# Kernel tuning notes

Hardware: AMD Instinct MI355X
Metric: run time of the kernel (lower is better)

## Reference

```python
import jax, jax.numpy as jnp
import numpy as np

N_NODES = 100000
N_EDGES = 3200000
IN_CH = 128
HID = 128
ACT_DIM = 1


def _gcn_layer(x, W, b, src, dst, ew, n):
    # GCNConv with edge weights and self-loops already included in (src, dst, ew).
    # Symmetric normalization: norm_e = d^{-1/2}[src] * w_e * d^{-1/2}[dst]
    h = x @ W                                            # [N, F_out] dense transform first (cheap)
    deg = jax.ops.segment_sum(ew, dst, num_segments=n)   # weighted in-degree
    dinv = jnp.where(deg > 0, jax.lax.rsqrt(deg), 0.0)
    norm = dinv[src] * ew * dinv[dst]                    # [E]
    out = jax.ops.segment_sum(norm[:, None] * h[src], dst, num_segments=n)
    return out + b


def setup_inputs() -> dict:
    key = jax.random.key(0)
    ks = jax.random.split(key, 10)
    x = jax.random.normal(ks[0], (N_NODES, IN_CH), dtype=jnp.float32)
    edge_index = jax.random.randint(ks[1], (2, N_EDGES), 0, N_NODES, dtype=jnp.int64)
    edge_weight = jax.random.uniform(ks[2], (N_EDGES,), dtype=jnp.float32)
    action = jax.random.normal(ks[3], (N_NODES, ACT_DIM), dtype=jnp.float32)
    s1 = 1.0 / np.sqrt(IN_CH)
    s2 = 1.0 / np.sqrt(HID)
    s3 = 1.0 / np.sqrt(HID + ACT_DIM)
    W1 = jax.random.uniform(ks[4], (IN_CH, HID), jnp.float32, -s1, s1)
    b1 = jnp.zeros((HID,), jnp.float32)
    W2 = jax.random.uniform(ks[5], (HID, HID), jnp.float32, -s2, s2)
    b2 = jnp.zeros((HID,), jnp.float32)
    Wfc = jax.random.uniform(ks[6], (HID + ACT_DIM, 1), jnp.float32, -s3, s3)
    bfc = jax.random.uniform(ks[7], (1,), jnp.float32, -s3, s3)
    return {"x": x, "edge_index": edge_index, "edge_weight": edge_weight,
            "action": action, "W1": W1, "b1": b1, "W2": W2, "b2": b2,
            "Wfc": Wfc, "bfc": bfc}


def reference(x, edge_index, edge_weight, action, W1, b1, W2, b2, Wfc, bfc):
    n = x.shape[0]
    loop = jnp.arange(n, dtype=edge_index.dtype)
    src = jnp.concatenate([edge_index[0], loop])          # add self-loops
    dst = jnp.concatenate([edge_index[1], loop])
    ew = jnp.concatenate([edge_weight, jnp.ones((n,), edge_weight.dtype)])

    h = jax.nn.relu(_gcn_layer(x, W1, b1, src, dst, ew, n))
    h = jax.nn.relu(_gcn_layer(h, W2, b2, src, dst, ew, n))
    h = jnp.concatenate([h, action], axis=1)              # [N, HID+ACT_DIM]
    value = (h @ Wfc + bfc).squeeze()                     # [N]
    return value
```

## Files before the change

kernel.cpp:

```cpp
#include <hip/hip_runtime.h>
#include <hip/hip_bf16.h>
#include <stdint.h>

typedef unsigned short u16;
typedef uint32_t u32;
typedef unsigned long long u64;

__device__ __forceinline__ float bf2f(u16 u) {
    return __uint_as_float(((uint32_t)u) << 16);
}
__device__ __forceinline__ u16 f2bf(float f) {
    uint32_t u = __float_as_uint(f);
    uint32_t r = u + 0x7fffu + ((u >> 16) & 1u);
    return (u16)(r >> 16);
}

__device__ __forceinline__ float ldf(const float* p) { return *p; }
__device__ __forceinline__ float ldf(const u16* p) { return bf2f(*p); }

#define DEG_SCALE 4294967296.0f
#define DEG_INV 2.3283064365386963e-10f

#define BSHIFT 9
#define BSIZE 512
#define CAP 19456

__global__ void k_init0(u32* bwptr, int NB) {
    int t = threadIdx.x;
    if (t < NB) bwptr[t] = (u32)t * CAP;
}

template <typename TIn>
__device__ __forceinline__ void gemm_block(float* smem, const TIn* __restrict__ A,
                                           const float* __restrict__ W,
                                           u16* __restrict__ outp, int n, int bid) {
    float (*As)[128] = (float(*)[128])smem;
    float (*Ws)[128] = (float(*)[128])(smem + 32 * 128);
    int t = threadIdx.x;
    int row0 = bid * 32;

    if constexpr (sizeof(TIn) == 2) {
        for (int i = t; i < 32 * 64; i += 256) {
            int r = i >> 6, c2 = i & 63;
            int gr = row0 + r;
            uint32_t u = (gr < n) ? *reinterpret_cast<const uint32_t*>(&A[(size_t)gr * 128 + 2 * c2]) : 0u;
            As[r][2 * c2] = bf2f((u16)(u & 0xffff));
            As[r][2 * c2 + 1] = bf2f((u16)(u >> 16));
        }
    } else {
        for (int i = t; i < 32 * 128; i += 256) {
            int r = i >> 7, c = i & 127;
            int gr = row0 + r;
            As[r][c] = (gr < n) ? ldf(&A[(size_t)gr * 128 + c]) : 0.0f;
        }
    }

    float acc[4][4];
#pragma unroll
    for (int i = 0; i < 4; i++)
#pragma unroll
        for (int j = 0; j < 4; j++) acc[i][j] = 0.0f;

    int c0 = (t & 31) * 4;
    int r0 = (t >> 5) * 4;

    for (int kt = 0; kt < 128; kt += 32) {
        __syncthreads();
        for (int i = t; i < 32 * 128; i += 256) {
            int kk = i >> 7, c = i & 127;
            Ws[kk][c] = W[(size_t)(kt + kk) * 128 + c];
        }
        __syncthreads();
#pragma unroll
        for (int kk = 0; kk < 32; kk += 4) {
            float w0[4], w1[4], w2[4], w3[4];
            *(float4*)w0 = *(const float4*)&Ws[kk + 0][c0];
            *(float4*)w1 = *(const float4*)&Ws[kk + 1][c0];
            *(float4*)w2 = *(const float4*)&Ws[kk + 2][c0];
            *(float4*)w3 = *(const float4*)&Ws[kk + 3][c0];
#pragma unroll
            for (int i = 0; i < 4; i++) {
                float a[4];
                *(float4*)a = *(const float4*)&As[r0 + i][kt + kk];
#pragma unroll
                for (int j = 0; j < 4; j++) {
                    acc[i][j] = fmaf(a[0], w0[j], acc[i][j]);
                    acc[i][j] = fmaf(a[1], w1[j], acc[i][j]);
                    acc[i][j] = fmaf(a[2], w2[j], acc[i][j]);
                    acc[i][j] = fmaf(a[3], w3[j], acc[i][j]);
                }
            }
        }
    }

#pragma unroll
    for (int i = 0; i < 4; i++) {
        int gr = row0 + r0 + i;
        if (gr < n) {
            ushort4 o;
            o.x = f2bf(acc[i][0]);
            o.y = f2bf(acc[i][1]);
            o.z = f2bf(acc[i][2]);
            o.w = f2bf(acc[i][3]);
            *reinterpret_cast<ushort4*>(&outp[(size_t)gr * 128 + c0]) = o;
        }
    }
}

__global__ __launch_bounds__(256) void k_part_gemm(const float* __restrict__ x, const float* __restrict__ W1,
                                                   u16* __restrict__ tbuf, int n, int Gg,
                                                   const int* __restrict__ src, const int* __restrict__ dst,
                                                   const float* __restrict__ ew,
                                                   u32* bwptr, u64* __restrict__ ebuf,
                                                   int E, int EPB, int NB) {
    __shared__ float smem[2 * 32 * 128];
    int bid = blockIdx.x;
    int g = bid / 5;
    int r = bid - g * 5;
    if (r < 3) {
        int gb = 3 * g + r;
        if (gb < Gg) gemm_block<float>(smem, x, W1, tbuf, n, gb);
        return;
    }
    int pb = 2 * g + (r - 3);
    u32* hist = (u32*)smem;
    u32* base = (u32*)smem + 256;
    int t = threadIdx.x;
    if (t < NB) hist[t] = 0;
    __syncthreads();
    int e0 = pb * EPB;
    int e1 = min(e0 + EPB, E);
    if (e0 >= E) return;
    for (int e = e0 + t; e < e1; e += 256) {
        atomicAdd(&hist[dst[e] >> BSHIFT], 1u);
    }
    __syncthreads();
    if (t < NB) {
        base[t] = atomicAdd(&bwptr[t], hist[t]);
        hist[t] = 0;
    }
    __syncthreads();
    for (int e = e0 + t; e < e1; e += 256) {
        int d = dst[e];
        int b = d >> BSHIFT;
        u32 pos = base[b] + atomicAdd(&hist[b], 1u);
        u32 w0 = (u32)src[e] | ((u32)(d & (BSIZE - 1)) << 17);
        ebuf[pos] = (u64)w0 | ((u64)__float_as_uint(ew[e]) << 32);
    }
}

__global__ __launch_bounds__(512) void k_bdegcnt(const u64* __restrict__ ebuf, const u32* __restrict__ bwptr,
                                                 u64* __restrict__ packed, int n) {
    __shared__ u64 acc[BSIZE];
    int b = blockIdx.x;
    int t = threadIdx.x;
    for (int i = t; i < BSIZE; i += 512) acc[i] = 0;
    __syncthreads();
    int cnt = (int)(bwptr[b] - (u32)b * CAP);
    const u64* eb = ebuf + (size_t)b * CAP;
    for (int e = t; e < cnt; e += 512) {
        u64 w = eb[e];
        int dlow = ((u32)w >> 17) & (BSIZE - 1);
        float wv = __uint_as_float((u32)(w >> 32));
        atomicAdd(&acc[dlow], (1ull << 48) | (u64)(wv * DEG_SCALE));
    }
    __syncthreads();
    int node0 = b << BSHIFT;
    for (int i = t; i < BSIZE; i += 512) {
        int node = node0 + i;
        if (node < n) packed[node] = acc[i] + (1ull << 32);
    }
}

__global__ void k_dinv_scan(const u64* __restrict__ packed, float* dinv, int* rowptr, int* bsum, int n) {
    __shared__ int s[256];
    int t = threadIdx.x;
    int i = blockIdx.x * 256 + t;
    u64 pk = (i < n) ? packed[i] : 0;
    if (i < n) {
        float deg = (float)(pk & 0xFFFFFFFFFFFFull) * DEG_INV;
        dinv[i] = rsqrtf(deg);
    }
    int v = (int)(pk >> 48);
    s[t] = v;
    __syncthreads();
    for (int off = 1; off < 256; off <<= 1) {
        int x = (t >= off) ? s[t - off] : 0;
        __syncthreads();
        s[t] += x;
        __syncthreads();
    }
    if (i < n) rowptr[i] = s[t] - v;
    if (t == 255) bsum[blockIdx.x] = s[255];
}

__global__ void k_scan_sums(int* bsum, int nb) {
    __shared__ int s[512];
    int t = threadIdx.x;
    int v = (t < nb) ? bsum[t] : 0;
    s[t] = v;
    __syncthreads();
    for (int off = 1; off < 512; off <<= 1) {
        int x = (t >= off) ? s[t - off] : 0;
        __syncthreads();
        s[t] += x;
        __syncthreads();
    }
    if (t < nb) bsum[t] = s[t] - v;
}

__global__ void k_scan_add(int* rowptr, const int* __restrict__ bsum, int n) {
    int i = blockIdx.x * 256 + threadIdx.x;
    if (i < n) rowptr[i] += bsum[blockIdx.x];
}

__global__ __launch_bounds__(512) void k_bscatter(const u64* __restrict__ ebuf, const u32* __restrict__ bwptr,
                                                  const int* __restrict__ rowptr, const float* __restrict__ dinv,
                                                  int2* __restrict__ rec, int n) {
    __shared__ u32 fill[BSIZE];
    __shared__ int rp[BSIZE];
    __shared__ float din[BSIZE];
    int b = blockIdx.x;
    int t = threadIdx.x;
    int node0 = b << BSHIFT;
    for (int i = t; i < BSIZE; i += 512) {
        int node = node0 + i;
        fill[i] = 0;
        rp[i] = (node < n) ? rowptr[node] : 0;
        din[i] = (node < n) ? dinv[node] : 0.f;
    }
    __syncthreads();
    int cnt = (int)(bwptr[b] - (u32)b * CAP);
    const u64* eb = ebuf + (size_t)b * CAP;
    for (int e = t; e < cnt; e += 512) {
        u64 w = eb[e];
        u32 lo = (u32)w;
        int s = lo & 0x1FFFF;
        int dlow = (lo >> 17) & (BSIZE - 1);
        float ewv = __uint_as_float((u32)(w >> 32));
        float nrm = dinv[s] * ewv * din[dlow];
        int pos = rp[dlow] + (int)atomicAdd(&fill[dlow], 1u);
        rec[pos] = make_int2(s, __float_as_int(nrm));
    }
}

template <typename TIn>
__global__ __launch_bounds__(256) void k_gemm(const TIn* __restrict__ A, const float* __restrict__ W,
                                              u16* __restrict__ outp, int n) {
    __shared__ float smem[2 * 32 * 128];
    gemm_block<TIn>(smem, A, W, outp, n, blockIdx.x);
}

template <int MODE>
__global__ __launch_bounds__(256) void k_agg(const u16* __restrict__ t, const int2* __restrict__ rec,
                                             const int* __restrict__ rowptr, const u64* __restrict__ packed,
                                             const float* __restrict__ dinv, const float* __restrict__ bias,
                                             u16* __restrict__ hout,
                                             const float* __restrict__ action, const float* __restrict__ Wfc,
                                             const float* __restrict__ bfc, float* __restrict__ out, int n) {
    int node = blockIdx.x * 4 + (threadIdx.x >> 6);
    if (node >= n) return;
    int lane = threadIdx.x & 63;
    int half = lane >> 5;
    int c4 = (lane & 31) * 4;
    int base = rowptr[node];
    int m = (int)(packed[node] >> 48);

    float4 acc = make_float4(0.f, 0.f, 0.f, 0.f);
    int e = 0;
    for (; e + 8 <= m; e += 8) {
        int2 r0 = rec[base + e + 0 + half];
        int2 r1 = rec[base + e + 2 + half];
        int2 r2 = rec[base + e + 4 + half];
        int2 r3 = rec[base + e + 6 + half];
        ushort4 g0 = *reinterpret_cast<const ushort4*>(&t[(size_t)r0.x * 128 + c4]);
        ushort4 g1 = *reinterpret_cast<const ushort4*>(&t[(size_t)r1.x * 128 + c4]);
        ushort4 g2 = *reinterpret_cast<const ushort4*>(&t[(size_t)r2.x * 128 + c4]);
        ushort4 g3 = *reinterpret_cast<const ushort4*>(&t[(size_t)r3.x * 128 + c4]);
        float n0 = __int_as_float(r0.y), n1 = __int_as_float(r1.y);
        float n2 = __int_as_float(r2.y), n3 = __int_as_float(r3.y);
        acc.x = fmaf(n0, bf2f(g0.x), acc.x); acc.y = fmaf(n0, bf2f(g0.y), acc.y);
        acc.z = fmaf(n0, bf2f(g0.z), acc.z); acc.w = fmaf(n0, bf2f(g0.w), acc.w);
        acc.x = fmaf(n1, bf2f(g1.x), acc.x); acc.y = fmaf(n1, bf2f(g1.y), acc.y);
        acc.z = fmaf(n1, bf2f(g1.z), acc.z); acc.w = fmaf(n1, bf2f(g1.w), acc.w);
        acc.x = fmaf(n2, bf2f(g2.x), acc.x); acc.y = fmaf(n2, bf2f(g2.y), acc.y);
        acc.z = fmaf(n2, bf2f(g2.z), acc.z); acc.w = fmaf(n2, bf2f(g2.w), acc.w);
        acc.x = fmaf(n3, bf2f(g3.x), acc.x); acc.y = fmaf(n3, bf2f(g3.y), acc.y);
        acc.z = fmaf(n3, bf2f(g3.z), acc.z); acc.w = fmaf(n3, bf2f(g3.w), acc.w);
    }
    for (; e + 2 <= m; e += 2) {
        int2 r = rec[base + e + half];
        ushort4 g = *reinterpret_cast<const ushort4*>(&t[(size_t)r.x * 128 + c4]);
        float nn = __int_as_float(r.y);
        acc.x = fmaf(nn, bf2f(g.x), acc.x); acc.y = fmaf(nn, bf2f(g.y), acc.y);
        acc.z = fmaf(nn, bf2f(g.z), acc.z); acc.w = fmaf(nn, bf2f(g.w), acc.w);
    }
    if (e < m && half == 0) {
        int2 r = rec[base + e];
        ushort4 g = *reinterpret_cast<const ushort4*>(&t[(size_t)r.x * 128 + c4]);
        float nn = __int_as_float(r.y);
        acc.x = fmaf(nn, bf2f(g.x), acc.x); acc.y = fmaf(nn, bf2f(g.y), acc.y);
        acc.z = fmaf(nn, bf2f(g.z), acc.z); acc.w = fmaf(nn, bf2f(g.w), acc.w);
    }
    acc.x += __shfl_xor(acc.x, 32);
    acc.y += __shfl_xor(acc.y, 32);
    acc.z += __shfl_xor(acc.z, 32);
    acc.w += __shfl_xor(acc.w, 32);

    if (half == 0) {
        float di = dinv[node];
        float sdi = di * di;
        ushort4 sv = *reinterpret_cast<const ushort4*>(&t[(size_t)node * 128 + c4]);
        acc.x = fmaf(sdi, bf2f(sv.x), acc.x);
        acc.y = fmaf(sdi, bf2f(sv.y), acc.y);
        acc.z = fmaf(sdi, bf2f(sv.z), acc.z);
        acc.w = fmaf(sdi, bf2f(sv.w), acc.w);
        float4 b = *reinterpret_cast<const float4*>(&bias[c4]);
        acc.x = fmaxf(acc.x + b.x, 0.0f);
        acc.y = fmaxf(acc.y + b.y, 0.0f);
        acc.z = fmaxf(acc.z + b.z, 0.0f);
        acc.w = fmaxf(acc.w + b.w, 0.0f);
        if (MODE == 0) {
            ushort4 o;
            o.x = f2bf(acc.x); o.y = f2bf(acc.y); o.z = f2bf(acc.z); o.w = f2bf(acc.w);
            *reinterpret_cast<ushort4*>(&hout[(size_t)node * 128 + c4]) = o;
        } else {
            float4 w = *reinterpret_cast<const float4*>(&Wfc[c4]);
            float v = acc.x * w.x + acc.y * w.y + acc.z * w.z + acc.w * w.w;
#pragma unroll
            for (int off = 16; off >= 1; off >>= 1) v += __shfl_down(v, off, 32);
            if (lane == 0) out[node] = v + action[node] * Wfc[128] + bfc[0];
        }
    }
}

extern "C" void kernel_launch(void* const* d_in, const int* in_sizes, int n_in,
                              void* d_out, int out_size, void* d_ws, size_t ws_size,
                              hipStream_t stream) {
    const float* x = (const float*)d_in[0];
    const int* ei = (const int*)d_in[1];
    const float* ew = (const float*)d_in[2];
    const float* action = (const float*)d_in[3];
    const float* W1 = (const float*)d_in[4];
    const float* b1 = (const float*)d_in[5];
    const float* W2 = (const float*)d_in[6];
    const float* b2 = (const float*)d_in[7];
    const float* Wfc = (const float*)d_in[8];
    const float* bfc = (const float*)d_in[9];
    float* out = (float*)d_out;

    int n = in_sizes[0] / 128;
    int E = in_sizes[2];
    const int* src = ei;
    const int* dst = ei + E;

    char* p = (char*)d_ws;
    auto carve = [&](size_t bytes) -> char* {
        char* q = p;
        p += (bytes + 255) & ~(size_t)255;
        return q;
    };
    int NB = (n + BSIZE - 1) >> BSHIFT;
    u64* packed = (u64*)carve((size_t)n * 8);
    float* dinv = (float*)carve((size_t)n * 4);
    int* rowptr = (int*)carve((size_t)n * 4);
    int* bsum = (int*)carve(1024 * 4);
    u32* bwptr = (u32*)carve((size_t)NB * 4);
    u64* ebuf = (u64*)carve((size_t)NB * CAP * 8);
    int2* rec = (int2*)carve(((size_t)E + 16) * 8);
    u16* tbuf = (u16*)carve((size_t)n * 128 * 2);
    u16* hbuf = (u16*)carve((size_t)n * 128 * 2);

    int nb = (n + 255) / 256;
    int Gg = (n + 31) / 32;
    int G = (Gg + 2) / 3;
    int Gp = 2 * G;
    int EPB = (E + Gp - 1) / Gp;

    k_init0<<<1, 256, 0, stream>>>(bwptr, NB);
    k_part_gemm<<<G * 5, 256, 0, stream>>>(x, W1, tbuf, n, Gg, src, dst, ew,
                                           bwptr, ebuf, E, EPB, NB);
    k_bdegcnt<<<NB, 512, 0, stream>>>(ebuf, bwptr, packed, n);
    k_dinv_scan<<<nb, 256, 0, stream>>>(packed, dinv, rowptr, bsum, n);
    k_scan_sums<<<1, 512, 0, stream>>>(bsum, nb);
    k_scan_add<<<nb, 256, 0, stream>>>(rowptr, bsum, n);
    k_bscatter<<<NB, 512, 0, stream>>>(ebuf, bwptr, rowptr, dinv, rec, n);

    k_agg<0><<<(n + 3) / 4, 256, 0, stream>>>(tbuf, rec, rowptr, packed, dinv, b1, hbuf,
                                              nullptr, nullptr, nullptr, nullptr, n);
    k_gemm<u16><<<(n + 31) / 32, 256, 0, stream>>>(hbuf, W2, tbuf, n);
    k_agg<1><<<(n + 3) / 4, 256, 0, stream>>>(tbuf, rec, rowptr, packed, dinv, b2, nullptr,
                                              action, Wfc, bfc, out, n);
}
```

Measured before the change: 561.3 us.

## Fuse degree count with per-bucket scan and widen aggregation gathers to 16 bytes

Every block of the partition kernel now does both a GEMM tile and an edge partition chunk, replacing the interleaved 3:2 block split. Degree counting, dinv and the rowptr scan are merged into one per-bucket kernel whose rowptr uses bucket-local offsets (b*CAP), so three scan kernels and the global prefix sum go away. The rec array is sized per bucket to match. The aggregation kernel now gives each lane 8 channels with 16-byte loads and processes 4 edges per step in parallel, which cuts the per-edge instruction count and the index-load overhead but adds a cross-lane reduction.

```diff
diff --git a/kernel.cpp b/kernel.cpp
--- a/kernel.cpp
+++ b/kernel.cpp
@@ -115,46 +115,45 @@
                                                    int E, int EPB, int NB) {
     __shared__ float smem[2 * 32 * 128];
     int bid = blockIdx.x;
-    int g = bid / 5;
-    int r = bid - g * 5;
-    if (r < 3) {
-        int gb = 3 * g + r;
-        if (gb < Gg) gemm_block<float>(smem, x, W1, tbuf, n, gb);
-        return;
-    }
-    int pb = 2 * g + (r - 3);
+    int t = threadIdx.x;
+
+    if (bid < Gg) gemm_block<float>(smem, x, W1, tbuf, n, bid);
+    __syncthreads();
+
     u32* hist = (u32*)smem;
     u32* base = (u32*)smem + 256;
-    int t = threadIdx.x;
     if (t < NB) hist[t] = 0;
     __syncthreads();
-    int e0 = pb * EPB;
+    int e0 = bid * EPB;
     int e1 = min(e0 + EPB, E);
-    if (e0 >= E) return;
-    for (int e = e0 + t; e < e1; e += 256) {
-        atomicAdd(&hist[dst[e] >> BSHIFT], 1u);
-    }
-    __syncthreads();
-    if (t < NB) {
-        base[t] = atomicAdd(&bwptr[t], hist[t]);
-        hist[t] = 0;
-    }
-    __syncthreads();
-    for (int e = e0 + t; e < e1; e += 256) {
-        int d = dst[e];
-        int b = d >> BSHIFT;
-        u32 pos = base[b] + atomicAdd(&hist[b], 1u);
-        u32 w0 = (u32)src[e] | ((u32)(d & (BSIZE - 1)) << 17);
-        ebuf[pos] = (u64)w0 | ((u64)__float_as_uint(ew[e]) << 32);
-    }
-}
-
-__global__ __launch_bounds__(512) void k_bdegcnt(const u64* __restrict__ ebuf, const u32* __restrict__ bwptr,
-                                                 u64* __restrict__ packed, int n) {
+    if (e0 < E) {
+        for (int e = e0 + t; e < e1; e += 256) {
+            atomicAdd(&hist[dst[e] >> BSHIFT], 1u);
+        }
+        __syncthreads();
+        if (t < NB) {
+            base[t] = atomicAdd(&bwptr[t], hist[t]);
+            hist[t] = 0;
+        }
+        __syncthreads();
+        for (int e = e0 + t; e < e1; e += 256) {
+            int d = dst[e];
+            int b = d >> BSHIFT;
+            u32 pos = base[b] + atomicAdd(&hist[b], 1u);
+            u32 w0 = (u32)src[e] | ((u32)(d & (BSIZE - 1)) << 17);
+            ebuf[pos] = (u64)w0 | ((u64)__float_as_uint(ew[e]) << 32);
+        }
+    }
+}
+
+__global__ __launch_bounds__(512) void k_bucket(const u64* __restrict__ ebuf, const u32* __restrict__ bwptr,
+                                                u64* __restrict__ packed, float* __restrict__ dinv,
+                                                int* __restrict__ rowptr, int n) {
     __shared__ u64 acc[BSIZE];
+    __shared__ int sc[BSIZE];
     int b = blockIdx.x;
     int t = threadIdx.x;
-    for (int i = t; i < BSIZE; i += 512) acc[i] = 0;
+    acc[t] = 0;
     __syncthreads();
     int cnt = (int)(bwptr[b] - (u32)b * CAP);
     const u64* eb = ebuf + (size_t)b * CAP;
@@ -165,53 +164,22 @@
         atomicAdd(&acc[dlow], (1ull << 48) | (u64)(wv * DEG_SCALE));
     }
     __syncthreads();
-    int node0 = b << BSHIFT;
-    for (int i = t; i < BSIZE; i += 512) {
-        int node = node0 + i;
-        if (node < n) packed[node] = acc[i] + (1ull << 32);
-    }
-}
-
-__global__ void k_dinv_scan(const u64* __restrict__ packed, float* dinv, int* rowptr, int* bsum, int n) {
-    __shared__ int s[256];
-    int t = threadIdx.x;
-    int i = blockIdx.x * 256 + t;
-    u64 pk = (i < n) ? packed[i] : 0;
-    if (i < n) {
-        float deg = (float)(pk & 0xFFFFFFFFFFFFull) * DEG_INV;
-        dinv[i] = rsqrtf(deg);
-    }
-    int v = (int)(pk >> 48);
-    s[t] = v;
-    __syncthreads();
-    for (int off = 1; off < 256; off <<= 1) {
-        int x = (t >= off) ? s[t - off] : 0;
-        __syncthreads();
-        s[t] += x;
-        __syncthreads();
-    }
-    if (i < n) rowptr[i] = s[t] - v;
-    if (t == 255) bsum[blockIdx.x] = s[255];
-}
-
-__global__ void k_scan_sums(int* bsum, int nb) {
-    __shared__ int s[512];
-    int t = threadIdx.x;
-    int v = (t < nb) ? bsum[t] : 0;
-    s[t] = v;
+    u64 pk = acc[t] + (1ull << 32);
+    int c = (int)(pk >> 48);
+    sc[t] = c;
     __syncthreads();
     for (int off = 1; off < 512; off <<= 1) {
-        int x = (t >= off) ? s[t - off] : 0;
-        __syncthreads();
-        s[t] += x;
-        __syncthreads();
-    }
-    if (t < nb) bsum[t] = s[t] - v;
-}
-
-__global__ void k_scan_add(int* rowptr, const int* __restrict__ bsum, int n) {
-    int i = blockIdx.x * 256 + threadIdx.x;
-    if (i < n) rowptr[i] += bsum[blockIdx.x];
+        int x = (t >= off) ? sc[t - off] : 0;
+        __syncthreads();
+        sc[t] += x;
+        __syncthreads();
+    }
+    int node = (b << BSHIFT) + t;
+    if (node < n) {
+        packed[node] = pk;
+        dinv[node] = rsqrtf((float)(pk & 0xFFFFFFFFFFFFull) * DEG_INV);
+        rowptr[node] = b * CAP + (sc[t] - c);
+    }
 }
 
 __global__ __launch_bounds__(512) void k_bscatter(const u64* __restrict__ ebuf, const u32* __restrict__ bwptr,
@@ -261,74 +229,78 @@
     int node = blockIdx.x * 4 + (threadIdx.x >> 6);
     if (node >= n) return;
     int lane = threadIdx.x & 63;
-    int half = lane >> 5;
-    int c4 = (lane & 31) * 4;
+    int sl = lane >> 4;
+    int c8 = (lane & 15) * 8;
     int base = rowptr[node];
     int m = (int)(packed[node] >> 48);
 
-    float4 acc = make_float4(0.f, 0.f, 0.f, 0.f);
-    int e = 0;
-    for (; e + 8 <= m; e += 8) {
-        int2 r0 = rec[base + e + 0 + half];
-        int2 r1 = rec[base + e + 2 + half];
-        int2 r2 = rec[base + e + 4 + half];
-        int2 r3 = rec[base + e + 6 + half];
-        ushort4 g0 = *reinterpret_cast<const ushort4*>(&t[(size_t)r0.x * 128 + c4]);
-        ushort4 g1 = *reinterpret_cast<const ushort4*>(&t[(size_t)r1.x * 128 + c4]);
-        ushort4 g2 = *reinterpret_cast<const ushort4*>(&t[(size_t)r2.x * 128 + c4]);
-        ushort4 g3 = *reinterpret_cast<const ushort4*>(&t[(size_t)r3.x * 128 + c4]);
-        float n0 = __int_as_float(r0.y), n1 = __int_as_float(r1.y);
-        float n2 = __int_as_float(r2.y), n3 = __int_as_float(r3.y);
-        acc.x = fmaf(n0, bf2f(g0.x), acc.x); acc.y = fmaf(n0, bf2f(g0.y), acc.y);
-        acc.z = fmaf(n0, bf2f(g0.z), acc.z); acc.w = fmaf(n0, bf2f(g0.w), acc.w);
-        acc.x = fmaf(n1, bf2f(g1.x), acc.x); acc.y = fmaf(n1, bf2f(g1.y), acc.y);
-        acc.z = fmaf(n1, bf2f(g1.z), acc.z); acc.w = fmaf(n1, bf2f(g1.w), acc.w);
-        acc.x = fmaf(n2, bf2f(g2.x), acc.x); acc.y = fmaf(n2, bf2f(g2.y), acc.y);
-        acc.z = fmaf(n2, bf2f(g2.z), acc.z); acc.w = fmaf(n2, bf2f(g2.w), acc.w);
-        acc.x = fmaf(n3, bf2f(g3.x), acc.x); acc.y = fmaf(n3, bf2f(g3.y), acc.y);
-        acc.z = fmaf(n3, bf2f(g3.z), acc.z); acc.w = fmaf(n3, bf2f(g3.w), acc.w);
-    }
-    for (; e + 2 <= m; e += 2) {
-        int2 r = rec[base + e + half];
-        ushort4 g = *reinterpret_cast<const ushort4*>(&t[(size_t)r.x * 128 + c4]);
-        float nn = __int_as_float(r.y);
-        acc.x = fmaf(nn, bf2f(g.x), acc.x); acc.y = fmaf(nn, bf2f(g.y), acc.y);
-        acc.z = fmaf(nn, bf2f(g.z), acc.z); acc.w = fmaf(nn, bf2f(g.w), acc.w);
-    }
-    if (e < m && half == 0) {
-        int2 r = rec[base + e];
-        ushort4 g = *reinterpret_cast<const ushort4*>(&t[(size_t)r.x * 128 + c4]);
-        float nn = __int_as_float(r.y);
-        acc.x = fmaf(nn, bf2f(g.x), acc.x); acc.y = fmaf(nn, bf2f(g.y), acc.y);
-        acc.z = fmaf(nn, bf2f(g.z), acc.z); acc.w = fmaf(nn, bf2f(g.w), acc.w);
-    }
-    acc.x += __shfl_xor(acc.x, 32);
-    acc.y += __shfl_xor(acc.y, 32);
-    acc.z += __shfl_xor(acc.z, 32);
-    acc.w += __shfl_xor(acc.w, 32);
-
-    if (half == 0) {
+    float a0 = 0.f, a1 = 0.f, a2 = 0.f, a3 = 0.f, a4 = 0.f, a5 = 0.f, a6 = 0.f, a7 = 0.f;
+
+#define ACCUM(G, NN)                                                         \
+    {                                                                        \
+        float nv = (NN);                                                     \
+        a0 = fmaf(nv, __uint_as_float((G).x << 16), a0);                     \
+        a1 = fmaf(nv, __uint_as_float((G).x & 0xFFFF0000u), a1);             \
+        a2 = fmaf(nv, __uint_as_float((G).y << 16), a2);                     \
+        a3 = fmaf(nv, __uint_as_float((G).y & 0xFFFF0000u), a3);             \
+        a4 = fmaf(nv, __uint_as_float((G).z << 16), a4);                     \
+        a5 = fmaf(nv, __uint_as_float((G).z & 0xFFFF0000u), a5);             \
+        a6 = fmaf(nv, __uint_as_float((G).w << 16), a6);                     \
+        a7 = fmaf(nv, __uint_as_float((G).w & 0xFFFF0000u), a7);             \
+    }
+
+    for (int e = 0; e < m; e += 8) {
+        int e0 = e + sl;
+        int e1 = e + 4 + sl;
+        int2 r0 = (e0 < m) ? rec[base + e0] : make_int2(0, 0);
+        int2 r1 = (e1 < m) ? rec[base + e1] : make_int2(0, 0);
+        uint4 g0 = *reinterpret_cast<const uint4*>(t + (((u32)r0.x << 7) + c8));
+        uint4 g1 = *reinterpret_cast<const uint4*>(t + (((u32)r1.x << 7) + c8));
+        ACCUM(g0, __int_as_float(r0.y));
+        ACCUM(g1, __int_as_float(r1.y));
+    }
+#undef ACCUM
+
+#define RED(A)                                   \
+    A += __shfl_xor(A, 16, 64);                  \
+    A += __shfl_xor(A, 32, 64);
+    RED(a0) RED(a1) RED(a2) RED(a3) RED(a4) RED(a5) RED(a6) RED(a7)
+#undef RED
+
+    if (sl == 0) {
         float di = dinv[node];
         float sdi = di * di;
-        ushort4 sv = *reinterpret_cast<const ushort4*>(&t[(size_t)node * 128 + c4]);
-        acc.x = fmaf(sdi, bf2f(sv.x), acc.x);
-        acc.y = fmaf(sdi, bf2f(sv.y), acc.y);
-        acc.z = fmaf(sdi, bf2f(sv.z), acc.z);
-        acc.w = fmaf(sdi, bf2f(sv.w), acc.w);
-        float4 b = *reinterpret_cast<const float4*>(&bias[c4]);
-        acc.x = fmaxf(acc.x + b.x, 0.0f);
-        acc.y = fmaxf(acc.y + b.y, 0.0f);
-        acc.z = fmaxf(acc.z + b.z, 0.0f);
-        acc.w = fmaxf(acc.w + b.w, 0.0f);
+        uint4 sv = *reinterpret_cast<const uint4*>(t + (((u32)node << 7) + c8));
+        a0 = fmaf(sdi, __uint_as_float(sv.x << 16), a0);
+        a1 = fmaf(sdi, __uint_as_float(sv.x & 0xFFFF0000u), a1);
+        a2 = fmaf(sdi, __uint_as_float(sv.y << 16), a2);
+        a3 = fmaf(sdi, __uint_as_float(sv.y & 0xFFFF0000u), a3);
+        a4 = fmaf(sdi, __uint_as_float(sv.z << 16), a4);
+        a5 = fmaf(sdi, __uint_as_float(sv.z & 0xFFFF0000u), a5);
+        a6 = fmaf(sdi, __uint_as_float(sv.w << 16), a6);
+        a7 = fmaf(sdi, __uint_as_float(sv.w & 0xFFFF0000u), a7);
+        float4 b0 = *reinterpret_cast<const float4*>(&bias[c8]);
+        float4 b1 = *reinterpret_cast<const float4*>(&bias[c8 + 4]);
+        a0 = fmaxf(a0 + b0.x, 0.f); a1 = fmaxf(a1 + b0.y, 0.f);
+        a2 = fmaxf(a2 + b0.z, 0.f); a3 = fmaxf(a3 + b0.w, 0.f);
+        a4 = fmaxf(a4 + b1.x, 0.f); a5 = fmaxf(a5 + b1.y, 0.f);
+        a6 = fmaxf(a6 + b1.z, 0.f); a7 = fmaxf(a7 + b1.w, 0.f);
         if (MODE == 0) {
-            ushort4 o;
-            o.x = f2bf(acc.x); o.y = f2bf(acc.y); o.z = f2bf(acc.z); o.w = f2bf(acc.w);
-            *reinterpret_cast<ushort4*>(&hout[(size_t)node * 128 + c4]) = o;
+            uint4 o;
+            o.x = (u32)f2bf(a0) | ((u32)f2bf(a1) << 16);
+            o.y = (u32)f2bf(a2) | ((u32)f2bf(a3) << 16);
+            o.z = (u32)f2bf(a4) | ((u32)f2bf(a5) << 16);
+            o.w = (u32)f2bf(a6) | ((u32)f2bf(a7) << 16);
+            *reinterpret_cast<uint4*>(hout + (((u32)node << 7) + c8)) = o;
         } else {
-            float4 w = *reinterpret_cast<const float4*>(&Wfc[c4]);
-            float v = acc.x * w.x + acc.y * w.y + acc.z * w.z + acc.w * w.w;
-#pragma unroll
-            for (int off = 16; off >= 1; off >>= 1) v += __shfl_down(v, off, 32);
+            float4 w0 = *reinterpret_cast<const float4*>(&Wfc[c8]);
+            float4 w1 = *reinterpret_cast<const float4*>(&Wfc[c8 + 4]);
+            float v = a0 * w0.x + a1 * w0.y + a2 * w0.z + a3 * w0.w +
+                      a4 * w1.x + a5 * w1.y + a6 * w1.z + a7 * w1.w;
+            v += __shfl_xor(v, 1, 64);
+            v += __shfl_xor(v, 2, 64);
+            v += __shfl_xor(v, 4, 64);
+            v += __shfl_xor(v, 8, 64);
             if (lane == 0) out[node] = v + action[node] * Wfc[128] + bfc[0];
         }
     }
@@ -364,31 +336,24 @@
     u64* packed = (u64*)carve((size_t)n * 8);
     float* dinv = (float*)carve((size_t)n * 4);
     int* rowptr = (int*)carve((size_t)n * 4);
-    int* bsum = (int*)carve(1024 * 4);
     u32* bwptr = (u32*)carve((size_t)NB * 4);
     u64* ebuf = (u64*)carve((size_t)NB * CAP * 8);
-    int2* rec = (int2*)carve(((size_t)E + 16) * 8);
+    int2* rec = (int2*)carve((size_t)NB * CAP * 8);
     u16* tbuf = (u16*)carve((size_t)n * 128 * 2);
     u16* hbuf = (u16*)carve((size_t)n * 128 * 2);
 
-    int nb = (n + 255) / 256;
     int Gg = (n + 31) / 32;
-    int G = (Gg + 2) / 3;
-    int Gp = 2 * G;
-    int EPB = (E + Gp - 1) / Gp;
+    int EPB = (E + Gg - 1) / Gg;
 
     k_init0<<<1, 256, 0, stream>>>(bwptr, NB);
-    k_part_gemm<<<G * 5, 256, 0, stream>>>(x, W1, tbuf, n, Gg, src, dst, ew,
-                                           bwptr, ebuf, E, EPB, NB);
-    k_bdegcnt<<<NB, 512, 0, stream>>>(ebuf, bwptr, packed, n);
-    k_dinv_scan<<<nb, 256, 0, stream>>>(packed, dinv, rowptr, bsum, n);
-    k_scan_sums<<<1, 512, 0, stream>>>(bsum, nb);
-    k_scan_add<<<nb, 256, 0, stream>>>(rowptr, bsum, n);
+    k_part_gemm<<<Gg, 256, 0, stream>>>(x, W1, tbuf, n, Gg, src, dst, ew,
+                                        bwptr, ebuf, E, EPB, NB);
+    k_bucket<<<NB, 512, 0, stream>>>(ebuf, bwptr, packed, dinv, rowptr, n);
     k_bscatter<<<NB, 512, 0, stream>>>(ebuf, bwptr, rowptr, dinv, rec, n);
 
     k_agg<0><<<(n + 3) / 4, 256, 0, stream>>>(tbuf, rec, rowptr, packed, dinv, b1, hbuf,
                                               nullptr, nullptr, nullptr, nullptr, n);
-    k_gemm<u16><<<(n + 31) / 32, 256, 0, stream>>>(hbuf, W2, tbuf, n);
+    k_gemm<u16><<<Gg, 256, 0, stream>>>(hbuf, W2, tbuf, n);
     k_agg<1><<<(n + 3) / 4, 256, 0, stream>>>(tbuf, rec, rowptr, packed, dinv, b2, nullptr,
                                               action, Wfc, bfc, out, n);
 }
```

After: 567.9 us. About the same (+1.2%).
